# Kernel optimization log

Hardware: AMD Instinct MI355X
Metric: run time of the kernel (lower is better)

Reference implementation:

```python
import jax, jax.numpy as jnp
import numpy as np

K = 3  # conv1d kernel size
PAD = (K - 1) // 2


def _conv1d_1ch(x, w, b):
    # x: (B, 1, C), w: (1, 1, K), b: (1,)  -- torch Conv1d cross-correlation
    c = x.shape[-1]
    xp = jnp.pad(x, ((0, 0), (0, 0), (PAD, PAD)))
    y = sum(w[0, 0, k] * xp[:, :, k:k + c] for k in range(K))
    return y + b[0]


def setup_inputs() -> dict:
    key = jax.random.key(0)
    ks = jax.random.split(key, 13)
    B, C, H, W, E = 8, 256, 48, 48, 64
    s = lambda fan: 1.0 / np.sqrt(fan)
    return {
        "feature": jax.random.normal(ks[0], (B, C, H, W), jnp.float32),
        "wq1": jax.random.normal(ks[1], (1, 1, K), jnp.float32) * s(K),
        "bq1": jax.random.normal(ks[2], (1,), jnp.float32) * s(K),
        "wk1": jax.random.normal(ks[3], (1, 1, K), jnp.float32) * s(K),
        "bk1": jax.random.normal(ks[4], (1,), jnp.float32) * s(K),
        "wq2": jax.random.normal(ks[5], (E, C), jnp.float32) * s(C),
        "bq2": jax.random.normal(ks[6], (E,), jnp.float32) * s(C),
        "wk2": jax.random.normal(ks[7], (E, C), jnp.float32) * s(C),
        "bk2": jax.random.normal(ks[8], (E,), jnp.float32) * s(C),
        "wv2": jax.random.normal(ks[9], (E, C), jnp.float32) * s(C),
        "bv2": jax.random.normal(ks[10], (E,), jnp.float32) * s(C),
        "watt": jax.random.normal(ks[11], (C, E), jnp.float32) * s(E),
        "batt": jax.random.normal(ks[12], (C,), jnp.float32) * s(E),
    }


def reference(feature, wq1, bq1, wk1, bk1, wq2, bq2, wk2, bk2, wv2, bv2, watt, batt):
    b, c, h, w = feature.shape
    hw = h * w

    # ---- Global Channel Attention ----
    gap = jnp.mean(feature, axis=(2, 3)).reshape(b, 1, c)
    query = jax.nn.sigmoid(_conv1d_1ch(gap, wq1, bq1))  # (b,1,c)
    key_ = jax.nn.sigmoid(_conv1d_1ch(gap, wk1, bk1))   # (b,1,c)
    att_c = key_[:, 0, :, None] * query[:, 0, None, :]  # (b,c,c) = K^T Q
    att_c = jax.nn.softmax(att_c, axis=1)               # softmax over dim=1
    value = feature.reshape(b, hw, c)                   # raw reshape, as in torch
    gc = jnp.matmul(value, att_c).reshape(b, c, h, w)   # raw reshape back

    # ---- Global Spatial Attention ----
    q = (jnp.einsum('bchw,ec->behw', feature, wq2) + bq2[None, :, None, None]).reshape(b, -1, hw)
    k = (jnp.einsum('bchw,ec->behw', feature, wk2) + bk2[None, :, None, None]).reshape(b, -1, hw)
    v = (jnp.einsum('bchw,ec->behw', feature, wv2) + bv2[None, :, None, None]).reshape(b, -1, hw)
    att_s = jnp.einsum('bei,bej->bij', k, q)            # (b,hw,hw)
    att_s = jax.nn.softmax(att_s, axis=2)
    gs = jnp.einsum('bei,bij->bej', v, att_s).reshape(b, -1, h, w)  # (b,e,h,w)
    gs = jnp.einsum('behw,ce->bchw', gs, watt) + batt[None, :, None, None]

    # ---- Gated combination ----
    feature_gc = feature * gc
    return feature_gc * gs + feature_gc
```

## Files before the change

### kernel.cpp

```cpp
#include <hip/hip_runtime.h>

#define B_ 8
#define C_ 256
#define HW_ 2304
#define E_ 64
#define SB_ (C_*HW_)

typedef unsigned short u16;
typedef __attribute__((ext_vector_type(8))) __bf16 bf16x8;
typedef __attribute__((ext_vector_type(4))) float f32x4;
#define MFMA16(a,b,c) __builtin_amdgcn_mfma_f32_16x16x32_bf16(a,b,c,0,0,0)

#define LDS_FENCE() do { asm volatile("s_waitcnt lgkmcnt(0)" ::: "memory"); \
                         __builtin_amdgcn_sched_barrier(0); } while(0)

static __device__ inline u16 f2bf(float x){
  unsigned u = __builtin_bit_cast(unsigned, x);
  u += 0x7FFFu + ((u >> 16) & 1u);
  return (u16)(u >> 16);
}
static __device__ inline float bf2f(u16 h){
  unsigned u = ((unsigned)h) << 16;
  return __builtin_bit_cast(float, u);
}


__global__ __launch_bounds__(256) void k_gap(const float* __restrict__ f, float* __restrict__ gap){
  int bc = blockIdx.x;
  const float* row = f + (size_t)bc * HW_;
  float s = 0.f;
  for (int i = threadIdx.x; i < HW_; i += 256) s += row[i];
  #pragma unroll
  for (int off = 32; off; off >>= 1) s += __shfl_down(s, off);
  __shared__ float red[4];
  int lane = threadIdx.x & 63, wv = threadIdx.x >> 6;
  if (lane == 0) red[wv] = s;
  __syncthreads();
  if (threadIdx.x == 0) gap[bc] = (red[0]+red[1]+red[2]+red[3]) * (1.0f/HW_);
}

__global__ __launch_bounds__(256) void k_attc2(const float* __restrict__ gap,
    const float* __restrict__ wq1, const float* __restrict__ bq1,
    const float* __restrict__ wk1, const float* __restrict__ bk1,
    u16* __restrict__ ath, u16* __restrict__ atl){
  int b = blockIdx.x >> 8;
  int j = blockIdx.x & 255;
  int i = threadIdx.x;
  const float* g = gap + b*C_;
  float gm1 = (i > 0)      ? g[i-1] : 0.f;
  float g0  = g[i];
  float gp1 = (i < C_-1)   ? g[i+1] : 0.f;
  float keyv = wk1[0]*gm1 + wk1[1]*g0 + wk1[2]*gp1 + bk1[0];
  keyv = 1.f/(1.f+__expf(-keyv));
  float qm1 = (j > 0)      ? g[j-1] : 0.f;
  float q0  = g[j];
  float qp1 = (j < C_-1)   ? g[j+1] : 0.f;
  float qv = wq1[0]*qm1 + wq1[1]*q0 + wq1[2]*qp1 + bq1[0];
  qv = 1.f/(1.f+__expf(-qv));
  float s = keyv * qv;
  __shared__ float red[256];
  red[i] = s; __syncthreads();
  for (int st = 128; st > 0; st >>= 1){ if (i < st) red[i] = fmaxf(red[i], red[i+st]); __syncthreads(); }
  float mx = red[0]; __syncthreads();
  float e = __expf(s - mx);
  red[i] = e; __syncthreads();
  for (int st = 128; st > 0; st >>= 1){ if (i < st) red[i] += red[i+st]; __syncthreads(); }
  float sum = red[0];
  float x = e / sum;
  u16 hb = f2bf(x);
  size_t o = (((size_t)b*16 + (j>>4))*8 + (i>>5))*512 + (((i&31)>>3)*16 + (j&15))*8 + (i&7);
  ath[o] = hb;
  atl[o] = f2bf(x - bf2f(hb));
}

__global__ __launch_bounds__(256) void k_wcvt(const float* __restrict__ wq,
    const float* __restrict__ wk, const float* __restrict__ wv,
    u16* __restrict__ wbh, u16* __restrict__ wbl){
  int n = blockIdx.x*256 + threadIdx.x;
  int mz = n >> 14; int idx = n & 16383;
  int e = idx >> 8, c = idx & 255;
  const float* w = (mz==0) ? wq : ((mz==1) ? wk : wv);
  float x = w[idx];
  u16 hb = f2bf(x);
  size_t widx = (((size_t)mz*4 + (e>>4))*8 + (c>>5))*512 + (((c&31)>>3)*16 + (e&15))*8 + (c&7);
  wbh[widx] = hb;
  wbl[widx] = f2bf(x - bf2f(hb));
}

__global__ __launch_bounds__(64) void k_proj5(const float* __restrict__ f,
    const u16* __restrict__ wbh, const u16* __restrict__ wbl,
    const float* __restrict__ bq, const float* __restrict__ bk, const float* __restrict__ bv,
    u16* __restrict__ qh, u16* __restrict__ qlo,
    u16* __restrict__ kh, u16* __restrict__ klo,
    u16* __restrict__ vh, u16* __restrict__ vlo){
  int b = blockIdx.x; int p0 = blockIdx.y*16; int mz = blockIdx.z;
  int lane = threadIdx.x; int l15 = lane & 15, g = lane >> 4;
  const float* fb = f + (size_t)b*SB_ + p0 + l15;
  const u16* wh = wbh + (size_t)mz*16384;
  const u16* wl = wbl + (size_t)mz*16384;
  const float* bi = (mz==0) ? bq : ((mz==1) ? bk : bv);
  f32x4 c1[4], c2[4], c3[4];
  #pragma unroll
  for (int m = 0; m < 4; m++){
    c1[m] = (f32x4){0.f,0.f,0.f,0.f};
    c2[m] = (f32x4){0.f,0.f,0.f,0.f};
    c3[m] = (f32x4){0.f,0.f,0.f,0.f};
  }
  for (int ks = 0; ks < 8; ks++){
    int cb = ks*32 + g*8;
    float fe[8];
    #pragma unroll
    for (int u = 0; u < 8; u++) fe[u] = fb[(size_t)(cb + u)*HW_];
    union { u16 u[8]; bf16x8 v; } FH, FL;
    #pragma unroll
    for (int u = 0; u < 8; u++){
      u16 hb = f2bf(fe[u]);
      FH.u[u] = hb;
      FL.u[u] = f2bf(fe[u] - bf2f(hb));
    }
    #pragma unroll
    for (int m = 0; m < 4; m++){
      bf16x8 awh = *(const bf16x8*)(wh + (m*8 + ks)*512 + lane*8);
      bf16x8 awl = *(const bf16x8*)(wl + (m*8 + ks)*512 + lane*8);
      c1[m] = MFMA16(awh, FH.v, c1[m]);
      c2[m] = MFMA16(awh, FL.v, c2[m]);
      c3[m] = MFMA16(awl, FH.v, c3[m]);
    }
  }
  if (mz < 2){
    u16* ohb = (mz==0 ? qh : kh);
    u16* olb = (mz==0 ? qlo: klo);
    size_t tb = ((size_t)b*144 + blockIdx.y)*2;
    #pragma unroll
    for (int m = 0; m < 4; m++){
      union { u16 u[4]; uint2 v2; } H, L;
      #pragma unroll
      for (int r = 0; r < 4; r++){
        int e = m*16 + g*4 + r;
        float x = c1[m][r] + c2[m][r] + c3[m][r] + bi[e];
        u16 hb = f2bf(x);
        H.u[r] = hb;
        L.u[r] = f2bf(x - bf2f(hb));
      }
      int kc = m >> 1;
      int gc = (m & 1)*2 + (g >> 1);
      int ub = (g & 1)*4;
      size_t idx = (tb + kc)*512 + (gc*16 + l15)*8 + ub;
      *(uint2*)(ohb + idx) = H.v2;
      *(uint2*)(olb + idx) = L.v2;
    }
  } else {
    int ic = blockIdx.y >> 1;
    int half = blockIdx.y & 1;
    int gg = half*2 + (l15 >> 3);
    int uu = l15 & 7;
    size_t vb0 = ((size_t)b*72 + ic)*4;
    #pragma unroll
    for (int m = 0; m < 4; m++){
      #pragma unroll
      for (int r = 0; r < 4; r++){
        int e = m*16 + g*4 + r;
        float x = c1[m][r] + c2[m][r] + c3[m][r] + bi[e];
        u16 hb = f2bf(x);
        size_t idx = (vb0 + m)*512 + (gg*16 + (g*4 + r))*8 + uu;
        vh[idx] = hb;
        vlo[idx] = f2bf(x - bf2f(hb));
      }
    }
  }
}

__global__ __launch_bounds__(64) void k_stats5(
    const u16* __restrict__ qh, const u16* __restrict__ qlo,
    const u16* __restrict__ kh, const u16* __restrict__ klo,
    float* __restrict__ lpart){
  int b = blockIdx.x; int jz = blockIdx.z;
  int lane = threadIdx.x; int l15 = lane & 15, g = lane >> 4;
  size_t kt = ((size_t)b*144 + blockIdx.y*2);
  bf16x8 kfh0[2], kfh1[2], kfl0[2], kfl1[2];
  #pragma unroll
  for (int isub = 0; isub < 2; isub++){
    kfh0[isub] = *(const bf16x8*)(kh  + ((kt+isub)*2 + 0)*512 + lane*8);
    kfh1[isub] = *(const bf16x8*)(kh  + ((kt+isub)*2 + 1)*512 + lane*8);
    kfl0[isub] = *(const bf16x8*)(klo + ((kt+isub)*2 + 0)*512 + lane*8);
    kfl1[isub] = *(const bf16x8*)(klo + ((kt+isub)*2 + 1)*512 + lane*8);
  }
  float lsum[8];
  #pragma unroll
  for (int x = 0; x < 8; x++) lsum[x] = 0.f;
  for (int jc = 0; jc < 9; jc++){
    #pragma unroll
    for (int nsub = 0; nsub < 2; nsub++){
      size_t qt = ((size_t)b*144 + jz*18 + jc*2 + nsub)*2;
      bf16x8 qf_h0 = *(const bf16x8*)(qh  + (qt+0)*512 + lane*8);
      bf16x8 qf_h1 = *(const bf16x8*)(qh  + (qt+1)*512 + lane*8);
      bf16x8 qf_l0 = *(const bf16x8*)(qlo + (qt+0)*512 + lane*8);
      bf16x8 qf_l1 = *(const bf16x8*)(qlo + (qt+1)*512 + lane*8);
      #pragma unroll
      for (int isub = 0; isub < 2; isub++){
        f32x4 c1 = {0.f,0.f,0.f,0.f}, c2 = {0.f,0.f,0.f,0.f}, c3 = {0.f,0.f,0.f,0.f};
        c1 = MFMA16(kfh0[isub], qf_h0, c1);
        c2 = MFMA16(kfh0[isub], qf_l0, c2);
        c3 = MFMA16(kfl0[isub], qf_h0, c3);
        c1 = MFMA16(kfh1[isub], qf_h1, c1);
        c2 = MFMA16(kfh1[isub], qf_l1, c2);
        c3 = MFMA16(kfl1[isub], qf_h1, c3);
        #pragma unroll
        for (int r = 0; r < 4; r++) lsum[isub*4+r] += __expf(c1[r] + c2[r] + c3[r]);
      }
    }
  }
  #pragma unroll
  for (int mk = 1; mk < 16; mk <<= 1){
    #pragma unroll
    for (int x = 0; x < 8; x++) lsum[x] += __shfl_xor(lsum[x], mk);
  }
  if (l15 == 0){
    float* lp = lpart + ((size_t)jz*B_ + b)*HW_ + blockIdx.y*32;
    #pragma unroll
    for (int isub = 0; isub < 2; isub++)
      #pragma unroll
      for (int r = 0; r < 4; r++) lp[isub*16 + g*4 + r] = lsum[isub*4+r];
  }
}

__global__ __launch_bounds__(256) void k_rl8(const float* __restrict__ lpart, float* __restrict__ rl){
  int i = blockIdx.x*256 + threadIdx.x;
  const int BH = B_*HW_;
  float s = 0.f;
  #pragma unroll
  for (int p = 0; p < 8; p++) s += lpart[(size_t)p*BH + i];
  rl[i] = 1.0f / s;
}

__global__ __launch_bounds__(64) void k_gs5(
    const u16* __restrict__ qh, const u16* __restrict__ qlo,
    const u16* __restrict__ kh, const u16* __restrict__ klo,
    const u16* __restrict__ vh, const u16* __restrict__ vlo,
    const float* __restrict__ rl, float* __restrict__ gsp){
  int b = blockIdx.x; int j0 = blockIdx.y*32; int iz = blockIdx.z;
  int lane = threadIdx.x; int l15 = lane & 15, g = lane >> 4;
  __shared__ __align__(16) u16 Ph[2][32][40];
  __shared__ __align__(16) u16 Pl[2][32][40];
  bf16x8 qfh0[2], qfh1[2], qfl0[2], qfl1[2];
  #pragma unroll
  for (int jt = 0; jt < 2; jt++){
    size_t qt = ((size_t)b*144 + blockIdx.y*2 + jt)*2;
    qfh0[jt] = *(const bf16x8*)(qh  + (qt+0)*512 + lane*8);
    qfh1[jt] = *(const bf16x8*)(qh  + (qt+1)*512 + lane*8);
    qfl0[jt] = *(const bf16x8*)(qlo + (qt+0)*512 + lane*8);
    qfl1[jt] = *(const bf16x8*)(qlo + (qt+1)*512 + lane*8);
  }
  f32x4 gacc[2][4];
  #pragma unroll
  for (int jt = 0; jt < 2; jt++)
    #pragma unroll
    for (int es = 0; es < 4; es++) gacc[jt][es] = (f32x4){0.f,0.f,0.f,0.f};
  const float* rlb = rl + b*HW_;
  for (int ic = 0; ic < 9; ic++){
    int i0c = iz*288 + ic*32;
    int buf = ic & 1;
    bf16x8 vfh[4], vfl[4];
    size_t vc = (((size_t)b*72 + iz*9 + ic)*4);
    #pragma unroll
    for (int es = 0; es < 4; es++){
      vfh[es] = *(const bf16x8*)(vh  + (vc+es)*512 + lane*8);
      vfl[es] = *(const bf16x8*)(vlo + (vc+es)*512 + lane*8);
    }
    #pragma unroll
    for (int msub = 0; msub < 2; msub++){
      size_t it = ((size_t)b*144 + iz*18 + ic*2 + msub)*2;
      bf16x8 kf_h0 = *(const bf16x8*)(kh  + (it+0)*512 + lane*8);
      bf16x8 kf_h1 = *(const bf16x8*)(kh  + (it+1)*512 + lane*8);
      bf16x8 kf_l0 = *(const bf16x8*)(klo + (it+0)*512 + lane*8);
      bf16x8 kf_l1 = *(const bf16x8*)(klo + (it+1)*512 + lane*8);
      f32x4 rlv = *(const f32x4*)&rlb[i0c + msub*16 + g*4];
      #pragma unroll
      for (int jt = 0; jt < 2; jt++){
        f32x4 c1 = {0.f,0.f,0.f,0.f}, c2 = {0.f,0.f,0.f,0.f}, c3 = {0.f,0.f,0.f,0.f};
        c1 = MFMA16(kf_h0, qfh0[jt], c1);
        c2 = MFMA16(kf_h0, qfl0[jt], c2);
        c3 = MFMA16(kf_l0, qfh0[jt], c3);
        c1 = MFMA16(kf_h1, qfh1[jt], c1);
        c2 = MFMA16(kf_h1, qfl1[jt], c2);
        c3 = MFMA16(kf_l1, qfh1[jt], c3);
        union { u16 u[4]; uint2 v2; } PH, PL;
        #pragma unroll
        for (int r = 0; r < 4; r++){
          float x = __expf(c1[r] + c2[r] + c3[r]) * rlv[r];
          u16 hb = f2bf(x);
          float hf = bf2f(hb);
          PH.u[r] = hb;
          PL.u[r] = f2bf(x - hf);
        }
        char* PhB = (char*)&Ph[buf][0][0] + (jt*16 + l15)*80 + msub*32 + g*8;
        char* PlB = (char*)&Pl[buf][0][0] + (jt*16 + l15)*80 + msub*32 + g*8;
        *(uint2*)PhB = PH.v2;
        *(uint2*)PlB = PL.v2;
      }
    }
    LDS_FENCE();
    #pragma unroll
    for (int jt = 0; jt < 2; jt++){
      bf16x8 pf_h = *(const bf16x8*)((char*)&Ph[buf][0][0] + (jt*16 + l15)*80 + g*16);
      bf16x8 pf_l = *(const bf16x8*)((char*)&Pl[buf][0][0] + (jt*16 + l15)*80 + g*16);
      #pragma unroll
      for (int es = 0; es < 4; es++){
        gacc[jt][es] = MFMA16(vfh[es], pf_h, gacc[jt][es]);
        gacc[jt][es] = MFMA16(vfh[es], pf_l, gacc[jt][es]);
        gacc[jt][es] = MFMA16(vfl[es], pf_h, gacc[jt][es]);
      }
    }
  }
  float* gb = gsp + ((size_t)iz*B_ + b)*E_*HW_;
  #pragma unroll
  for (int jt = 0; jt < 2; jt++)
    #pragma unroll
    for (int es = 0; es < 4; es++)
      #pragma unroll
      for (int r = 0; r < 4; r++){
        int e = es*16 + g*4 + r;
        gb[(size_t)e*HW_ + j0 + jt*16 + l15] = gacc[jt][es][r];
      }
}

__global__ __launch_bounds__(256) void k_gsum8(const float* __restrict__ gsp, float* __restrict__ gs){
  const size_t N = (size_t)B_*E_*HW_;
  size_t n = ((size_t)blockIdx.x*256 + threadIdx.x)*4;
  f32x4 s = *(const f32x4*)(gsp + n);
  #pragma unroll
  for (int p = 1; p < 8; p++) s += *(const f32x4*)(gsp + (size_t)p*N + n);
  *(f32x4*)(gs + n) = s;
}

__global__ __launch_bounds__(256) void k_gsout2(const float* __restrict__ gs,
    const float* __restrict__ watt, const float* __restrict__ batt,
    float* __restrict__ gsout){
  int b = blockIdx.x; int sc = blockIdx.y; int cc0 = blockIdx.z * 16;
  int s = sc*256 + threadIdx.x;
  const float* gb = gs + (size_t)b*E_*HW_ + s;
  float acc[16];
  #pragma unroll
  for (int x = 0; x < 16; x++) acc[x] = 0.f;
  for (int e = 0; e < E_; e++){
    float gv = gb[(size_t)e*HW_];
    #pragma unroll
    for (int x = 0; x < 16; x++) acc[x] += watt[(cc0+x)*E_ + e] * gv;
  }
  float* ob = gsout + (size_t)b*SB_ + (size_t)cc0*HW_ + s;
  #pragma unroll
  for (int x = 0; x < 16; x++) ob[(size_t)x*HW_] = acc[x] + batt[cc0 + x];
}

__global__ __launch_bounds__(64) void k_final2(const float* __restrict__ f,
    const u16* __restrict__ ath, const u16* __restrict__ atl,
    float* __restrict__ inout){
  int b = blockIdx.x; int s0 = blockIdx.y*16; int z = blockIdx.z;
  int lane = threadIdx.x; int l15 = lane & 15, g = lane >> 4;
  const float* fb = f + (size_t)b*SB_;
  bf16x8 Ah[8], Al[8];
  const float* arow = fb + (size_t)(s0 + l15)*C_;
  #pragma unroll
  for (int ks = 0; ks < 8; ks++){
    int cbase = ks*32 + g*8;
    float fe[8];
    #pragma unroll
    for (int e = 0; e < 8; e++) fe[e] = arow[cbase + e];
    union { u16 u[8]; bf16x8 v; } H, L;
    #pragma unroll
    for (int e = 0; e < 8; e++){
      u16 hb = f2bf(fe[e]);
      H.u[e] = hb;
      L.u[e] = f2bf(fe[e] - bf2f(hb));
    }
    Ah[ks] = H.v; Al[ks] = L.v;
  }
  const u16* abz_h = ath + (size_t)b*65536;
  const u16* abz_l = atl + (size_t)b*65536;
  f32x4 acc[8];
  #pragma unroll
  for (int q = 0; q < 8; q++) acc[q] = (f32x4){0.f,0.f,0.f,0.f};
  #pragma unroll
  for (int q = 0; q < 8; q++){
    int jt = z*8 + q;
    #pragma unroll
    for (int ks = 0; ks < 8; ks++){
      bf16x8 Bh = *(const bf16x8*)(abz_h + (jt*8 + ks)*512 + lane*8);
      bf16x8 Bl = *(const bf16x8*)(abz_l + (jt*8 + ks)*512 + lane*8);
      acc[q] = MFMA16(Ah[ks], Bh, acc[q]);
      acc[q] = MFMA16(Ah[ks], Bl, acc[q]);
      acc[q] = MFMA16(Al[ks], Bh, acc[q]);
    }
  }
  float* ob = inout + (size_t)b*SB_;
  #pragma unroll
  for (int q = 0; q < 8; q++){
    #pragma unroll
    for (int r = 0; r < 4; r++){
      int p = s0 + g*4 + r;
      int j = (z*8+q)*16 + l15;
      size_t n = (size_t)p*C_ + j;
      float fx = fb[n];
      float gso = ob[n];
      ob[n] = acc[q][r] * fx * (gso + 1.f);
    }
  }
}

extern "C" void kernel_launch(void* const* d_in, const int* in_sizes, int n_in,
                              void* d_out, int out_size, void* d_ws, size_t ws_size,
                              hipStream_t stream){
  const float* f    = (const float*)d_in[0];
  const float* wq1  = (const float*)d_in[1];
  const float* bq1  = (const float*)d_in[2];
  const float* wk1  = (const float*)d_in[3];
  const float* bk1  = (const float*)d_in[4];
  const float* wq2  = (const float*)d_in[5];
  const float* bq2  = (const float*)d_in[6];
  const float* wk2  = (const float*)d_in[7];
  const float* bk2  = (const float*)d_in[8];
  const float* wv2  = (const float*)d_in[9];
  const float* bv2  = (const float*)d_in[10];
  const float* watt = (const float*)d_in[11];
  const float* batt = (const float*)d_in[12];
  float* out = (float*)d_out;
  char* W = (char*)d_ws;

  float* gap   = (float*)(W + 0);
  u16*   ath   = (u16*)  (W + 8192);
  u16*   atl   = (u16*)  (W + 1056768);
  float* lpart = (float*)(W + 2105344);
  float* rl    = (float*)(W + 2695168);
  float* gsp   = (float*)(W + 2768896);
  float* gs    = (float*)(W + 40517632);
  u16* qh  = (u16*)(W + 45236224);
  u16* qlo = (u16*)(W + 47595520);
  u16* kh  = (u16*)(W + 49954816);
  u16* klo = (u16*)(W + 52314112);
  u16* vh  = (u16*)(W + 54673408);
  u16* vlo = (u16*)(W + 57032704);
  u16* wbh = (u16*)(W + 59392000);
  u16* wbl = (u16*)(W + 59490304);

  k_gap   <<<B_*C_,             256, 0, stream>>>(f, gap);
  k_attc2 <<<B_*C_,             256, 0, stream>>>(gap, wq1, bq1, wk1, bk1, ath, atl);
  k_wcvt  <<<192,               256, 0, stream>>>(wq2, wk2, wv2, wbh, wbl);
  k_proj5 <<<dim3(B_, 144, 3),   64, 0, stream>>>(f, wbh, wbl, bq2, bk2, bv2,
                                                  qh, qlo, kh, klo, vh, vlo);
  k_stats5<<<dim3(B_, 72, 8),    64, 0, stream>>>(qh, qlo, kh, klo, lpart);
  k_rl8   <<<B_*HW_/256,        256, 0, stream>>>(lpart, rl);
  k_gs5   <<<dim3(B_, 72, 8),    64, 0, stream>>>(qh, qlo, kh, klo, vh, vlo, rl, gsp);
  k_gsum8 <<<B_*E_*HW_/1024,    256, 0, stream>>>(gsp, gs);
  k_gsout2<<<dim3(B_, 9, 16),   256, 0, stream>>>(gs, watt, batt, out);
  k_final2<<<dim3(B_, 144, 2),   64, 0, stream>>>(f, ath, atl, out);
}
```

Before: 179.5 us.

## Rebalance grid splits across projection, stats, attention and final kernels; prefetch K fragments

Splits the QKV projection over two half-E blocks and the final channel-attention GEMM over four column groups, so more small blocks run. The spatial stats kernel now uses 9 j-partitions with fully unrolled tiles, and the attention-value kernel uses 6 i-partitions, which shrinks the partial-sum buffer and the reduction pass. The attention-value kernel also prefetches the next K fragments into registers and writes its output through LDS for coalesced vector stores. These changes trade more launch parallelism and latency hiding for higher register pressure and more redundant fragment loads.

```diff
diff --git a/kernel.cpp b/kernel.cpp
--- a/kernel.cpp
+++ b/kernel.cpp
@@ -24,6 +24,18 @@
   return __builtin_bit_cast(float, u);
 }
 
+
+struct KFrag { bf16x8 h0, h1, l0, l1; };
+static __device__ __forceinline__ KFrag ldfrag(const u16* __restrict__ ph,
+                                               const u16* __restrict__ pl,
+                                               size_t tile, int lane){
+  KFrag q;
+  q.h0 = *(const bf16x8*)(ph + (tile*2+0)*512 + (size_t)lane*8);
+  q.h1 = *(const bf16x8*)(ph + (tile*2+1)*512 + (size_t)lane*8);
+  q.l0 = *(const bf16x8*)(pl + (tile*2+0)*512 + (size_t)lane*8);
+  q.l1 = *(const bf16x8*)(pl + (tile*2+1)*512 + (size_t)lane*8);
+  return q;
+}
 
 __global__ __launch_bounds__(256) void k_gap(const float* __restrict__ f, float* __restrict__ gap){
   int bc = blockIdx.x;
@@ -87,25 +99,27 @@
   wbl[widx] = f2bf(x - bf2f(hb));
 }
 
-__global__ __launch_bounds__(64) void k_proj5(const float* __restrict__ f,
+__global__ __launch_bounds__(64) void k_proj6(const float* __restrict__ f,
     const u16* __restrict__ wbh, const u16* __restrict__ wbl,
     const float* __restrict__ bq, const float* __restrict__ bk, const float* __restrict__ bv,
     u16* __restrict__ qh, u16* __restrict__ qlo,
     u16* __restrict__ kh, u16* __restrict__ klo,
     u16* __restrict__ vh, u16* __restrict__ vlo){
-  int b = blockIdx.x; int p0 = blockIdx.y*16; int mz = blockIdx.z;
+  int b = blockIdx.x; int p0 = blockIdx.y*16;
+  int mz = blockIdx.z >> 1, mh = blockIdx.z & 1;
   int lane = threadIdx.x; int l15 = lane & 15, g = lane >> 4;
   const float* fb = f + (size_t)b*SB_ + p0 + l15;
   const u16* wh = wbh + (size_t)mz*16384;
   const u16* wl = wbl + (size_t)mz*16384;
   const float* bi = (mz==0) ? bq : ((mz==1) ? bk : bv);
-  f32x4 c1[4], c2[4], c3[4];
-  #pragma unroll
-  for (int m = 0; m < 4; m++){
+  f32x4 c1[2], c2[2], c3[2];
+  #pragma unroll
+  for (int m = 0; m < 2; m++){
     c1[m] = (f32x4){0.f,0.f,0.f,0.f};
     c2[m] = (f32x4){0.f,0.f,0.f,0.f};
     c3[m] = (f32x4){0.f,0.f,0.f,0.f};
   }
+  #pragma unroll
   for (int ks = 0; ks < 8; ks++){
     int cb = ks*32 + g*8;
     float fe[8];
@@ -119,12 +133,13 @@
       FL.u[u] = f2bf(fe[u] - bf2f(hb));
     }
     #pragma unroll
-    for (int m = 0; m < 4; m++){
-      bf16x8 awh = *(const bf16x8*)(wh + (m*8 + ks)*512 + lane*8);
-      bf16x8 awl = *(const bf16x8*)(wl + (m*8 + ks)*512 + lane*8);
-      c1[m] = MFMA16(awh, FH.v, c1[m]);
-      c2[m] = MFMA16(awh, FL.v, c2[m]);
-      c3[m] = MFMA16(awl, FH.v, c3[m]);
+    for (int ml = 0; ml < 2; ml++){
+      int m = mh*2 + ml;
+      bf16x8 awh = *(const bf16x8*)(wh + ((size_t)m*8 + ks)*512 + (size_t)lane*8);
+      bf16x8 awl = *(const bf16x8*)(wl + ((size_t)m*8 + ks)*512 + (size_t)lane*8);
+      c1[ml] = MFMA16(awh, FH.v, c1[ml]);
+      c2[ml] = MFMA16(awh, FL.v, c2[ml]);
+      c3[ml] = MFMA16(awl, FH.v, c3[ml]);
     }
   }
   if (mz < 2){
@@ -132,18 +147,19 @@
     u16* olb = (mz==0 ? qlo: klo);
     size_t tb = ((size_t)b*144 + blockIdx.y)*2;
     #pragma unroll
-    for (int m = 0; m < 4; m++){
+    for (int ml = 0; ml < 2; ml++){
+      int m = mh*2 + ml;
       union { u16 u[4]; uint2 v2; } H, L;
       #pragma unroll
       for (int r = 0; r < 4; r++){
         int e = m*16 + g*4 + r;
-        float x = c1[m][r] + c2[m][r] + c3[m][r] + bi[e];
+        float x = c1[ml][r] + c2[ml][r] + c3[ml][r] + bi[e];
         u16 hb = f2bf(x);
         H.u[r] = hb;
         L.u[r] = f2bf(x - bf2f(hb));
       }
-      int kc = m >> 1;
-      int gc = (m & 1)*2 + (g >> 1);
+      int kc = mh;
+      int gc = ml*2 + (g >> 1);
       int ub = (g & 1)*4;
       size_t idx = (tb + kc)*512 + (gc*16 + l15)*8 + ub;
       *(uint2*)(ohb + idx) = H.v2;
@@ -156,11 +172,12 @@
     int uu = l15 & 7;
     size_t vb0 = ((size_t)b*72 + ic)*4;
     #pragma unroll
-    for (int m = 0; m < 4; m++){
+    for (int ml = 0; ml < 2; ml++){
+      int m = mh*2 + ml;
       #pragma unroll
       for (int r = 0; r < 4; r++){
         int e = m*16 + g*4 + r;
-        float x = c1[m][r] + c2[m][r] + c3[m][r] + bi[e];
+        float x = c1[ml][r] + c2[ml][r] + c3[ml][r] + bi[e];
         u16 hb = f2bf(x);
         size_t idx = (vb0 + m)*512 + (gg*16 + (g*4 + r))*8 + uu;
         vh[idx] = hb;
@@ -170,44 +187,34 @@
   }
 }
 
-__global__ __launch_bounds__(64) void k_stats5(
+__global__ __launch_bounds__(64,2) void k_stats6(
     const u16* __restrict__ qh, const u16* __restrict__ qlo,
     const u16* __restrict__ kh, const u16* __restrict__ klo,
     float* __restrict__ lpart){
-  int b = blockIdx.x; int jz = blockIdx.z;
+  int b = blockIdx.x; int it0 = blockIdx.y; int jz = blockIdx.z;
   int lane = threadIdx.x; int l15 = lane & 15, g = lane >> 4;
-  size_t kt = ((size_t)b*144 + blockIdx.y*2);
-  bf16x8 kfh0[2], kfh1[2], kfl0[2], kfl1[2];
-  #pragma unroll
-  for (int isub = 0; isub < 2; isub++){
-    kfh0[isub] = *(const bf16x8*)(kh  + ((kt+isub)*2 + 0)*512 + lane*8);
-    kfh1[isub] = *(const bf16x8*)(kh  + ((kt+isub)*2 + 1)*512 + lane*8);
-    kfl0[isub] = *(const bf16x8*)(klo + ((kt+isub)*2 + 0)*512 + lane*8);
-    kfl1[isub] = *(const bf16x8*)(klo + ((kt+isub)*2 + 1)*512 + lane*8);
-  }
+  const size_t b144 = (size_t)b*144;
+  KFrag kf0 = ldfrag(kh, klo, b144 + it0*2,     lane);
+  KFrag kf1 = ldfrag(kh, klo, b144 + it0*2 + 1, lane);
   float lsum[8];
   #pragma unroll
   for (int x = 0; x < 8; x++) lsum[x] = 0.f;
-  for (int jc = 0; jc < 9; jc++){
-    #pragma unroll
-    for (int nsub = 0; nsub < 2; nsub++){
-      size_t qt = ((size_t)b*144 + jz*18 + jc*2 + nsub)*2;
-      bf16x8 qf_h0 = *(const bf16x8*)(qh  + (qt+0)*512 + lane*8);
-      bf16x8 qf_h1 = *(const bf16x8*)(qh  + (qt+1)*512 + lane*8);
-      bf16x8 qf_l0 = *(const bf16x8*)(qlo + (qt+0)*512 + lane*8);
-      bf16x8 qf_l1 = *(const bf16x8*)(qlo + (qt+1)*512 + lane*8);
-      #pragma unroll
-      for (int isub = 0; isub < 2; isub++){
-        f32x4 c1 = {0.f,0.f,0.f,0.f}, c2 = {0.f,0.f,0.f,0.f}, c3 = {0.f,0.f,0.f,0.f};
-        c1 = MFMA16(kfh0[isub], qf_h0, c1);
-        c2 = MFMA16(kfh0[isub], qf_l0, c2);
-        c3 = MFMA16(kfl0[isub], qf_h0, c3);
-        c1 = MFMA16(kfh1[isub], qf_h1, c1);
-        c2 = MFMA16(kfh1[isub], qf_l1, c2);
-        c3 = MFMA16(kfl1[isub], qf_h1, c3);
-        #pragma unroll
-        for (int r = 0; r < 4; r++) lsum[isub*4+r] += __expf(c1[r] + c2[r] + c3[r]);
-      }
+  size_t qb0 = b144 + jz*16;
+  #pragma unroll
+  for (int t = 0; t < 16; t++){
+    KFrag q = ldfrag(qh, qlo, qb0 + t, lane);
+    #pragma unroll
+    for (int isub = 0; isub < 2; isub++){
+      const KFrag& kf = isub ? kf1 : kf0;
+      f32x4 c1 = {0.f,0.f,0.f,0.f}, c2 = {0.f,0.f,0.f,0.f}, c3 = {0.f,0.f,0.f,0.f};
+      c1 = MFMA16(kf.h0, q.h0, c1);
+      c2 = MFMA16(kf.h0, q.l0, c2);
+      c3 = MFMA16(kf.l0, q.h0, c3);
+      c1 = MFMA16(kf.h1, q.h1, c1);
+      c2 = MFMA16(kf.h1, q.l1, c2);
+      c3 = MFMA16(kf.l1, q.h1, c3);
+      #pragma unroll
+      for (int r = 0; r < 4; r++) lsum[isub*4+r] += __expf(c1[r] + c2[r] + c3[r]);
     }
   }
   #pragma unroll
@@ -216,7 +223,7 @@
     for (int x = 0; x < 8; x++) lsum[x] += __shfl_xor(lsum[x], mk);
   }
   if (l15 == 0){
-    float* lp = lpart + ((size_t)jz*B_ + b)*HW_ + blockIdx.y*32;
+    float* lp = lpart + ((size_t)jz*B_ + b)*HW_ + it0*32;
     #pragma unroll
     for (int isub = 0; isub < 2; isub++)
       #pragma unroll
@@ -224,66 +231,66 @@
   }
 }
 
-__global__ __launch_bounds__(256) void k_rl8(const float* __restrict__ lpart, float* __restrict__ rl){
+__global__ __launch_bounds__(256) void k_rl9(const float* __restrict__ lpart, float* __restrict__ rl){
   int i = blockIdx.x*256 + threadIdx.x;
   const int BH = B_*HW_;
   float s = 0.f;
   #pragma unroll
-  for (int p = 0; p < 8; p++) s += lpart[(size_t)p*BH + i];
+  for (int p = 0; p < 9; p++) s += lpart[(size_t)p*BH + i];
   rl[i] = 1.0f / s;
 }
 
-__global__ __launch_bounds__(64) void k_gs5(
+__global__ __launch_bounds__(64,2) void k_gs6(
     const u16* __restrict__ qh, const u16* __restrict__ qlo,
     const u16* __restrict__ kh, const u16* __restrict__ klo,
     const u16* __restrict__ vh, const u16* __restrict__ vlo,
     const float* __restrict__ rl, float* __restrict__ gsp){
-  int b = blockIdx.x; int j0 = blockIdx.y*32; int iz = blockIdx.z;
+  int b = blockIdx.x; int jt0 = blockIdx.y; int iz = blockIdx.z;
+  int j0 = jt0*32;
   int lane = threadIdx.x; int l15 = lane & 15, g = lane >> 4;
-  __shared__ __align__(16) u16 Ph[2][32][40];
-  __shared__ __align__(16) u16 Pl[2][32][40];
-  bf16x8 qfh0[2], qfh1[2], qfl0[2], qfl1[2];
-  #pragma unroll
-  for (int jt = 0; jt < 2; jt++){
-    size_t qt = ((size_t)b*144 + blockIdx.y*2 + jt)*2;
-    qfh0[jt] = *(const bf16x8*)(qh  + (qt+0)*512 + lane*8);
-    qfh1[jt] = *(const bf16x8*)(qh  + (qt+1)*512 + lane*8);
-    qfl0[jt] = *(const bf16x8*)(qlo + (qt+0)*512 + lane*8);
-    qfl1[jt] = *(const bf16x8*)(qlo + (qt+1)*512 + lane*8);
-  }
+  __shared__ __align__(16) char smem[10240];
+  const size_t b144 = (size_t)b*144;
+  KFrag qf0 = ldfrag(qh, qlo, b144 + jt0*2,     lane);
+  KFrag qf1 = ldfrag(qh, qlo, b144 + jt0*2 + 1, lane);
   f32x4 gacc[2][4];
   #pragma unroll
   for (int jt = 0; jt < 2; jt++)
     #pragma unroll
     for (int es = 0; es < 4; es++) gacc[jt][es] = (f32x4){0.f,0.f,0.f,0.f};
   const float* rlb = rl + b*HW_;
-  for (int ic = 0; ic < 9; ic++){
-    int i0c = iz*288 + ic*32;
-    int buf = ic & 1;
+  KFrag kcur0 = ldfrag(kh, klo, b144 + (size_t)iz*24,     lane);
+  KFrag kcur1 = ldfrag(kh, klo, b144 + (size_t)iz*24 + 1, lane);
+  #pragma unroll
+  for (int ic = 0; ic < 12; ic++){
+    int i0c = iz*384 + ic*32;
+    KFrag kn0 = kcur0, kn1 = kcur1;
+    if (ic < 11){
+      kn0 = ldfrag(kh, klo, b144 + (size_t)iz*24 + (ic+1)*2,     lane);
+      kn1 = ldfrag(kh, klo, b144 + (size_t)iz*24 + (ic+1)*2 + 1, lane);
+    }
     bf16x8 vfh[4], vfl[4];
-    size_t vc = (((size_t)b*72 + iz*9 + ic)*4);
+    size_t vc = ((size_t)b*72 + iz*12 + ic)*4;
     #pragma unroll
     for (int es = 0; es < 4; es++){
-      vfh[es] = *(const bf16x8*)(vh  + (vc+es)*512 + lane*8);
-      vfl[es] = *(const bf16x8*)(vlo + (vc+es)*512 + lane*8);
-    }
+      vfh[es] = *(const bf16x8*)(vh  + (vc+es)*512 + (size_t)lane*8);
+      vfl[es] = *(const bf16x8*)(vlo + (vc+es)*512 + (size_t)lane*8);
+    }
+    char* PhB = smem + (ic & 1)*2560;
+    char* PlB = smem + 5120 + (ic & 1)*2560;
     #pragma unroll
     for (int msub = 0; msub < 2; msub++){
-      size_t it = ((size_t)b*144 + iz*18 + ic*2 + msub)*2;
-      bf16x8 kf_h0 = *(const bf16x8*)(kh  + (it+0)*512 + lane*8);
-      bf16x8 kf_h1 = *(const bf16x8*)(kh  + (it+1)*512 + lane*8);
-      bf16x8 kf_l0 = *(const bf16x8*)(klo + (it+0)*512 + lane*8);
-      bf16x8 kf_l1 = *(const bf16x8*)(klo + (it+1)*512 + lane*8);
+      const KFrag& kf = msub ? kcur1 : kcur0;
       f32x4 rlv = *(const f32x4*)&rlb[i0c + msub*16 + g*4];
       #pragma unroll
       for (int jt = 0; jt < 2; jt++){
+        const KFrag& qf = jt ? qf1 : qf0;
         f32x4 c1 = {0.f,0.f,0.f,0.f}, c2 = {0.f,0.f,0.f,0.f}, c3 = {0.f,0.f,0.f,0.f};
-        c1 = MFMA16(kf_h0, qfh0[jt], c1);
-        c2 = MFMA16(kf_h0, qfl0[jt], c2);
-        c3 = MFMA16(kf_l0, qfh0[jt], c3);
-        c1 = MFMA16(kf_h1, qfh1[jt], c1);
-        c2 = MFMA16(kf_h1, qfl1[jt], c2);
-        c3 = MFMA16(kf_l1, qfh1[jt], c3);
+        c1 = MFMA16(kf.h0, qf.h0, c1);
+        c2 = MFMA16(kf.h0, qf.l0, c2);
+        c3 = MFMA16(kf.l0, qf.h0, c3);
+        c1 = MFMA16(kf.h1, qf.h1, c1);
+        c2 = MFMA16(kf.h1, qf.l1, c2);
+        c3 = MFMA16(kf.l1, qf.h1, c3);
         union { u16 u[4]; uint2 v2; } PH, PL;
         #pragma unroll
         for (int r = 0; r < 4; r++){
@@ -293,17 +300,15 @@
           PH.u[r] = hb;
           PL.u[r] = f2bf(x - hf);
         }
-        char* PhB = (char*)&Ph[buf][0][0] + (jt*16 + l15)*80 + msub*32 + g*8;
-        char* PlB = (char*)&Pl[buf][0][0] + (jt*16 + l15)*80 + msub*32 + g*8;
-        *(uint2*)PhB = PH.v2;
-        *(uint2*)PlB = PL.v2;
+        *(uint2*)(PhB + (jt*16 + l15)*80 + msub*32 + g*8) = PH.v2;
+        *(uint2*)(PlB + (jt*16 + l15)*80 + msub*32 + g*8) = PL.v2;
       }
     }
     LDS_FENCE();
     #pragma unroll
     for (int jt = 0; jt < 2; jt++){
-      bf16x8 pf_h = *(const bf16x8*)((char*)&Ph[buf][0][0] + (jt*16 + l15)*80 + g*16);
-      bf16x8 pf_l = *(const bf16x8*)((char*)&Pl[buf][0][0] + (jt*16 + l15)*80 + g*16);
+      bf16x8 pf_h = *(const bf16x8*)(PhB + (jt*16 + l15)*80 + g*16);
+      bf16x8 pf_l = *(const bf16x8*)(PlB + (jt*16 + l15)*80 + g*16);
       #pragma unroll
       for (int es = 0; es < 4; es++){
         gacc[jt][es] = MFMA16(vfh[es], pf_h, gacc[jt][es]);
@@ -311,25 +316,34 @@
         gacc[jt][es] = MFMA16(vfl[es], pf_h, gacc[jt][es]);
       }
     }
-  }
+    kcur0 = kn0; kcur1 = kn1;
+  }
+  LDS_FENCE();
+  float* GT = (float*)smem;
+  #pragma unroll
+  for (int jt = 0; jt < 2; jt++)
+    #pragma unroll
+    for (int es = 0; es < 4; es++)
+      #pragma unroll
+      for (int r = 0; r < 4; r++)
+        GT[(es*16 + g*4 + r)*32 + jt*16 + l15] = gacc[jt][es][r];
+  LDS_FENCE();
   float* gb = gsp + ((size_t)iz*B_ + b)*E_*HW_;
   #pragma unroll
-  for (int jt = 0; jt < 2; jt++)
-    #pragma unroll
-    for (int es = 0; es < 4; es++)
-      #pragma unroll
-      for (int r = 0; r < 4; r++){
-        int e = es*16 + g*4 + r;
-        gb[(size_t)e*HW_ + j0 + jt*16 + l15] = gacc[jt][es][r];
-      }
-}
-
-__global__ __launch_bounds__(256) void k_gsum8(const float* __restrict__ gsp, float* __restrict__ gs){
+  for (int itx = 0; itx < 8; itx++){
+    int n = (itx*64 + lane)*4;
+    f32x4 vv = *(const f32x4*)&GT[n];
+    int e = n >> 5, jj = n & 31;
+    *(f32x4*)&gb[(size_t)e*HW_ + j0 + jj] = vv;
+  }
+}
+
+__global__ __launch_bounds__(256) void k_gsum6(const float* __restrict__ gsp, float* __restrict__ gs){
   const size_t N = (size_t)B_*E_*HW_;
   size_t n = ((size_t)blockIdx.x*256 + threadIdx.x)*4;
   f32x4 s = *(const f32x4*)(gsp + n);
   #pragma unroll
-  for (int p = 1; p < 8; p++) s += *(const f32x4*)(gsp + (size_t)p*N + n);
+  for (int p = 1; p < 6; p++) s += *(const f32x4*)(gsp + (size_t)p*N + n);
   *(f32x4*)(gs + n) = s;
 }
 
@@ -352,7 +366,7 @@
   for (int x = 0; x < 16; x++) ob[(size_t)x*HW_] = acc[x] + batt[cc0 + x];
 }
 
-__global__ __launch_bounds__(64) void k_final2(const float* __restrict__ f,
+__global__ __launch_bounds__(64,2) void k_final3(const float* __restrict__ f,
     const u16* __restrict__ ath, const u16* __restrict__ atl,
     float* __restrict__ inout){
   int b = blockIdx.x; int s0 = blockIdx.y*16; int z = blockIdx.z;
@@ -377,16 +391,16 @@
   }
   const u16* abz_h = ath + (size_t)b*65536;
   const u16* abz_l = atl + (size_t)b*65536;
-  f32x4 acc[8];
-  #pragma unroll
-  for (int q = 0; q < 8; q++) acc[q] = (f32x4){0.f,0.f,0.f,0.f};
-  #pragma unroll
-  for (int q = 0; q < 8; q++){
-    int jt = z*8 + q;
+  f32x4 acc[4];
+  #pragma unroll
+  for (int q = 0; q < 4; q++) acc[q] = (f32x4){0.f,0.f,0.f,0.f};
+  #pragma unroll
+  for (int q = 0; q < 4; q++){
+    int jt = z*4 + q;
     #pragma unroll
     for (int ks = 0; ks < 8; ks++){
-      bf16x8 Bh = *(const bf16x8*)(abz_h + (jt*8 + ks)*512 + lane*8);
-      bf16x8 Bl = *(const bf16x8*)(abz_l + (jt*8 + ks)*512 + lane*8);
+      bf16x8 Bh = *(const bf16x8*)(abz_h + ((size_t)jt*8 + ks)*512 + (size_t)lane*8);
+      bf16x8 Bl = *(const bf16x8*)(abz_l + ((size_t)jt*8 + ks)*512 + (size_t)lane*8);
       acc[q] = MFMA16(Ah[ks], Bh, acc[q]);
       acc[q] = MFMA16(Ah[ks], Bl, acc[q]);
       acc[q] = MFMA16(Al[ks], Bh, acc[q]);
@@ -394,11 +408,11 @@
   }
   float* ob = inout + (size_t)b*SB_;
   #pragma unroll
-  for (int q = 0; q < 8; q++){
+  for (int q = 0; q < 4; q++){
     #pragma unroll
     for (int r = 0; r < 4; r++){
       int p = s0 + g*4 + r;
-      int j = (z*8+q)*16 + l15;
+      int j = (z*4+q)*16 + l15;
       size_t n = (size_t)p*C_ + j;
       float fx = fb[n];
       float gso = ob[n];
@@ -430,27 +444,27 @@
   u16*   ath   = (u16*)  (W + 8192);
   u16*   atl   = (u16*)  (W + 1056768);
   float* lpart = (float*)(W + 2105344);
-  float* rl    = (float*)(W + 2695168);
-  float* gsp   = (float*)(W + 2768896);
-  float* gs    = (float*)(W + 40517632);
-  u16* qh  = (u16*)(W + 45236224);
-  u16* qlo = (u16*)(W + 47595520);
-  u16* kh  = (u16*)(W + 49954816);
-  u16* klo = (u16*)(W + 52314112);
-  u16* vh  = (u16*)(W + 54673408);
-  u16* vlo = (u16*)(W + 57032704);
-  u16* wbh = (u16*)(W + 59392000);
-  u16* wbl = (u16*)(W + 59490304);
+  float* rl    = (float*)(W + 4759552);
+  float* gsp   = (float*)(W + 4833280);
+  float* gs    = (float*)(W + 33144832);
+  u16* qh  = (u16*)(W + 37863424);
+  u16* qlo = (u16*)(W + 40222720);
+  u16* kh  = (u16*)(W + 42582016);
+  u16* klo = (u16*)(W + 44941312);
+  u16* vh  = (u16*)(W + 47300608);
+  u16* vlo = (u16*)(W + 49659904);
+  u16* wbh = (u16*)(W + 52019200);
+  u16* wbl = (u16*)(W + 52117504);
 
   k_gap   <<<B_*C_,             256, 0, stream>>>(f, gap);
   k_attc2 <<<B_*C_,             256, 0, stream>>>(gap, wq1, bq1, wk1, bk1, ath, atl);
   k_wcvt  <<<192,               256, 0, stream>>>(wq2, wk2, wv2, wbh, wbl);
-  k_proj5 <<<dim3(B_, 144, 3),   64, 0, stream>>>(f, wbh, wbl, bq2, bk2, bv2,
+  k_proj6 <<<dim3(B_, 144, 6),   64, 0, stream>>>(f, wbh, wbl, bq2, bk2, bv2,
                                                   qh, qlo, kh, klo, vh, vlo);
-  k_stats5<<<dim3(B_, 72, 8),    64, 0, stream>>>(qh, qlo, kh, klo, lpart);
-  k_rl8   <<<B_*HW_/256,        256, 0, stream>>>(lpart, rl);
-  k_gs5   <<<dim3(B_, 72, 8),    64, 0, stream>>>(qh, qlo, kh, klo, vh, vlo, rl, gsp);
-  k_gsum8 <<<B_*E_*HW_/1024,    256, 0, stream>>>(gsp, gs);
+  k_stats6<<<dim3(B_, 72, 9),    64, 0, stream>>>(qh, qlo, kh, klo, lpart);
+  k_rl9   <<<B_*HW_/256,        256, 0, stream>>>(lpart, rl);
+  k_gs6   <<<dim3(B_, 72, 6),    64, 0, stream>>>(qh, qlo, kh, klo, vh, vlo, rl, gsp);
+  k_gsum6 <<<B_*E_*HW_/1024,    256, 0, stream>>>(gsp, gs);
   k_gsout2<<<dim3(B_, 9, 16),   256, 0, stream>>>(gs, watt, batt, out);
-  k_final2<<<dim3(B_, 144, 2),   64, 0, stream>>>(f, ath, atl, out);
-}
+  k_final3<<<dim3(B_, 144, 4),   64, 0, stream>>>(f, ath, atl, out);
+}
```

New measurement: 162.4 us. 9.5% less time.
